# Optimization experiments

Measured on AMD Instinct MI355X. Metric: run time of the kernel, lower is better.

## Reference

```python
import jax, jax.numpy as jnp
import numpy as np

N = 100000
E = 1600000
DIN = 128
DOUT = 128
NUM_STEPS = 3


def setup_inputs() -> dict:
    key = jax.random.key(0)
    ks = jax.random.split(key, 12)
    stdv = 1.0 / np.sqrt(DOUT)
    xav = np.sqrt(6.0 / (2 * DOUT + DOUT))  # xavier_uniform for [DOUT, 2*DOUT]
    return {
        "input": jax.random.normal(ks[0], (N, DIN), dtype=jnp.float32),
        "edge_row": jax.random.randint(ks[1], (E,), 0, N, dtype=jnp.int32),
        "edge_col": jax.random.randint(ks[2], (E,), 0, N, dtype=jnp.int32),
        "edge_weight": jax.random.uniform(ks[3], (E,), dtype=jnp.float32),
        "weight": jax.random.uniform(ks[4], (DIN, DOUT), jnp.float32, -stdv, stdv),
        "bias": jax.random.uniform(ks[5], (DOUT,), jnp.float32, -stdv, stdv),
        "candidate_weight": jax.random.uniform(ks[6], (DOUT, DOUT), jnp.float32, -stdv, stdv),
        "ug_W": jax.random.uniform(ks[7], (DOUT, 2 * DOUT), jnp.float32, -xav, xav),
        "ug_b": jnp.zeros((DOUT,), jnp.float32),
        "rg_W": jax.random.uniform(ks[8], (DOUT, 2 * DOUT), jnp.float32, -xav, xav),
        "rg_b": jnp.zeros((DOUT,), jnp.float32),
    }


def reference(input, edge_row, edge_col, edge_weight, weight, bias,
              candidate_weight, ug_W, ug_b, rg_W, rg_b):
    n = input.shape[0]
    # h = input @ W + b
    h = input @ weight + bias
    for _ in range(NUM_STEPS):
        # spmm: m[dst] += w_e * h[src]
        msg = edge_weight[:, None] * h[edge_col]          # [E, DOUT]
        m = jax.ops.segment_sum(msg, edge_row, num_segments=n)  # [N, DOUT]
        g = jnp.concatenate([h, m], axis=1)               # [N, 2*DOUT]
        z = jax.nn.sigmoid(g @ ug_W.T + ug_b)
        r = jax.nn.sigmoid(g @ rg_W.T + rg_b)
        cand = jnp.tanh((r * h) @ candidate_weight)
        h = z * h + (1.0 - z) * cand
    return h
```

## Files before the change

kernel.cpp:

```cpp
#include <hip/hip_runtime.h>
#include <math.h>

#define NN 100000
#define EE 1600000
#define D 128
#define NBK 782
#define SBLK 128
#define EPB 12500
#define CAP 2304
#define EMAX 2048
#define INITB 3125

typedef __attribute__((ext_vector_type(8))) short short8;
typedef __attribute__((ext_vector_type(4))) float floatx4;

static __device__ __forceinline__ unsigned short f2bf(float f) {
  unsigned int u = __builtin_bit_cast(unsigned int, f);
  u = (u + 0x7fff + ((u >> 16) & 1)) >> 16;
  return (unsigned short)u;
}
static __device__ __forceinline__ unsigned int pk2(float a, float b) {
  return (unsigned int)f2bf(a) | ((unsigned int)f2bf(b) << 16);
}
static __device__ __forceinline__ float bflo(unsigned int u) { return __builtin_bit_cast(float, u << 16); }
static __device__ __forceinline__ float bfhi(unsigned int u) { return __builtin_bit_cast(float, u & 0xffff0000u); }
static __device__ __forceinline__ float bf2f(unsigned short s) {
  return __builtin_bit_cast(float, (unsigned int)s << 16);
}
static __device__ __forceinline__ float sig_f(float x) { return 1.f / (1.f + __expf(-x)); }
static __device__ __forceinline__ float tanh_f(float x) {
  float e = __expf(2.f * x);
  return 1.f - 2.f / (e + 1.f);
}
static __device__ __forceinline__ void fma8(float* acc, float w, uint4 h) {
  acc[0] += w * bflo(h.x); acc[1] += w * bfhi(h.x);
  acc[2] += w * bflo(h.y); acc[3] += w * bfhi(h.y);
  acc[4] += w * bflo(h.z); acc[5] += w * bfhi(h.z);
  acc[6] += w * bflo(h.w); acc[7] += w * bfhi(h.w);
}

__global__ __launch_bounds__(1024) void scatterpack(
    const int* __restrict__ erow, const int* __restrict__ ecol, const float* __restrict__ ew,
    int* __restrict__ len, int2* __restrict__ arena,
    const float* __restrict__ ugW, const float* __restrict__ rgW,
    const float* __restrict__ CW, const float* __restrict__ W,
    unsigned int* __restrict__ packZR, unsigned int* __restrict__ packCW,
    unsigned int* __restrict__ packW) {
  __shared__ int cur[NBK];
  const int tid = threadIdx.x;
  if (blockIdx.x < SBLK) {
    for (int b = tid; b < NBK; b += 1024) cur[b] = 0;
    __syncthreads();
    const int base = blockIdx.x * EPB;
    int r[13];
#pragma unroll
    for (int i = 0; i < 13; ++i) {
      int li = i * 1024 + tid;
      r[i] = (li < EPB) ? erow[base + li] : -1;
      if (r[i] >= 0) atomicAdd(&cur[r[i] >> 7], 1);
    }
    __syncthreads();
    for (int b = tid; b < NBK; b += 1024) {
      int c = cur[b];
      cur[b] = c ? (b * CAP + atomicAdd(&len[b], c)) : 0;
    }
    __syncthreads();
#pragma unroll
    for (int i = 0; i < 13; ++i) {
      if (r[i] >= 0) {
        int li = base + i * 1024 + tid;
        int pos = atomicAdd(&cur[r[i] >> 7], 1);
        int2 v;
        v.x = ecol[li] | ((r[i] & 127) << 24);
        v.y = __builtin_bit_cast(int, ew[li]);
        arena[pos] = v;
      }
    }
  } else {
    int g = (blockIdx.x - SBLK) * 16 + (tid >> 6);
    int lane = tid & 63;
    if (g < 128) {
      int nt = g >> 3, ks = g & 7;
      int o = nt * 16 + (lane & 15);
      int c0 = ks * 32 + (lane >> 4) * 8;
      const float* src = (o < 128 ? ugW + (size_t)o * 256 : rgW + (size_t)(o - 128) * 256) + c0;
      float4 f0 = ((const float4*)src)[0];
      float4 f1 = ((const float4*)src)[1];
      uint4 out;
      out.x = pk2(f0.x, f0.y);
      out.y = pk2(f0.z, f0.w);
      out.z = pk2(f1.x, f1.y);
      out.w = pk2(f1.z, f1.w);
      ((uint4*)packZR)[g * 64 + lane] = out;
    } else if (g < 192) {
      const float* M = (g < 160) ? CW : W;
      unsigned int* dst = (g < 160) ? packCW : packW;
      int gg = (g < 160) ? (g - 128) : (g - 160);
      int nt = gg >> 2, ks = gg & 3;
      int n = nt * 16 + (lane & 15);
      int k0 = ks * 32 + (lane >> 4) * 8;
      unsigned short v[8];
#pragma unroll
      for (int j = 0; j < 8; ++j) v[j] = f2bf(M[(size_t)(k0 + j) * 128 + n]);
      uint4 out;
      out.x = (unsigned int)v[0] | ((unsigned int)v[1] << 16);
      out.y = (unsigned int)v[2] | ((unsigned int)v[3] << 16);
      out.z = (unsigned int)v[4] | ((unsigned int)v[5] << 16);
      out.w = (unsigned int)v[6] | ((unsigned int)v[7] << 16);
      ((uint4*)dst)[gg * 64 + lane] = out;
    }
  }
}

__global__ __launch_bounds__(256) void sortinit(
    const int* __restrict__ len, int2* __restrict__ arena,
    int* __restrict__ row_start, int* __restrict__ row_end,
    const float* __restrict__ X, const short* __restrict__ packW, const float* __restrict__ bias,
    unsigned short* __restrict__ h_bf) {
  __shared__ __align__(16) char smem[CAP * 8 + 1024];
  const int tid = threadIdx.x;

  if (blockIdx.x < NBK) {
    int2* sE = (int2*)smem;
    int* rcnt = (int*)(smem + CAP * 8);
    int* rcur = rcnt + 128;
    const int b = blockIdx.x;
    const int lo = b * CAP;
    int n = len[b];
    n = (n < CAP) ? n : CAP;

    if (tid < 128) rcnt[tid] = 0;
    for (int i = tid; i < n; i += 256) sE[i] = arena[lo + i];
    __syncthreads();
    for (int i = tid; i < n; i += 256) atomicAdd(&rcnt[(sE[i].x >> 24) & 127], 1);
    __syncthreads();
    int myc = (tid < 128) ? rcnt[tid] : 0;
    for (int d = 1; d < 128; d <<= 1) {
      int v = (tid < 128 && tid >= d) ? rcnt[tid - d] : 0;
      __syncthreads();
      if (tid < 128) rcnt[tid] += v;
      __syncthreads();
    }
    if (tid < 128) {
      int excl = rcnt[tid] - myc;
      rcur[tid] = excl;
      int gr = b * 128 + tid;
      if (gr < NN) { row_start[gr] = lo + excl; row_end[gr] = lo + excl + myc; }
    }
    __syncthreads();
    for (int i = tid; i < n; i += 256) {
      int2 v = sE[i];
      int rl = (v.x >> 24) & 127;
      int pos = atomicAdd(&rcur[rl], 1);
      int2 o;
      o.x = v.x & 0x00FFFFFF;
      o.y = v.y;
      arena[lo + pos] = o;
    }
  } else {
    short* sX = (short*)smem;
    const int row0 = (blockIdx.x - NBK) * 32;

    {
      int r = tid >> 3, ch = tid & 7;
      const float4* px = (const float4*)(X + (size_t)(row0 + r) * D + ch * 16);
      float4 f0 = px[0], f1 = px[1], f2 = px[2], f3 = px[3];
      uint4 o0, o1;
      o0.x = pk2(f0.x, f0.y); o0.y = pk2(f0.z, f0.w);
      o0.z = pk2(f1.x, f1.y); o0.w = pk2(f1.z, f1.w);
      o1.x = pk2(f2.x, f2.y); o1.y = pk2(f2.z, f2.w);
      o1.z = pk2(f3.x, f3.y); o1.w = pk2(f3.z, f3.w);
      *(uint4*)(sX + r * 136 + ch * 16) = o0;
      *(uint4*)(sX + r * 136 + ch * 16 + 8) = o1;
    }
    __syncthreads();

    const int wave = tid >> 6, lane = tid & 63;
    const int quad = lane >> 4, l15 = lane & 15;
    const int mh = wave & 1, nh = wave >> 1;
    const int mrow = mh * 16 + l15;

    floatx4 acc[4];
    const floatx4 zero4 = {0.f, 0.f, 0.f, 0.f};
#pragma unroll
    for (int t = 0; t < 4; ++t) acc[t] = zero4;

    const short8* pW = (const short8*)packW;
#pragma unroll
    for (int ks = 0; ks < 4; ++ks) {
      short8 a = *(const short8*)(sX + mrow * 136 + ks * 32 + quad * 8);
#pragma unroll
      for (int t = 0; t < 4; ++t) {
        short8 b = pW[((nh * 4 + t) * 4 + ks) * 64 + lane];
        acc[t] = __builtin_amdgcn_mfma_f32_16x16x32_bf16(a, b, acc[t], 0, 0, 0);
      }
    }

    __syncthreads();
#pragma unroll
    for (int t = 0; t < 4; ++t) {
      int col = nh * 64 + t * 16 + l15;
      float bv = bias[col];
#pragma unroll
      for (int reg = 0; reg < 4; ++reg) {
        int row = mh * 16 + quad * 4 + reg;
        sX[row * 136 + col] = (short)f2bf(acc[t][reg] + bv);
      }
    }
    __syncthreads();
    for (int idx = tid; idx < 512; idx += 256) {
      int r = idx >> 4, ch = idx & 15;
      *(uint4*)(h_bf + (size_t)(row0 + r) * D + ch * 8) = *(uint4*)(sX + r * 136 + ch * 8);
    }
  }
}

__global__ __launch_bounds__(512, 8) void fused_step(
    const int* __restrict__ row_start, const int* __restrict__ row_end,
    const int2* __restrict__ edata,
    const uint4* __restrict__ h4,
    const short* __restrict__ packZR, const short* __restrict__ packCW,
    const float* __restrict__ ugb, const float* __restrict__ rgb,
    unsigned short* __restrict__ h_bf_out, float* __restrict__ h_f32_out, int last) {
  __shared__ __align__(16) short sA[32 * 264];
  __shared__ __align__(16) char sU[EMAX * 8];
  int2* sE = (int2*)sU;
  short* sRH = (short*)sU;

  const int tid = threadIdx.x;
  const int row0 = blockIdx.x * 32;
  const int wave = tid >> 6, lane = tid & 63;
  const int sub = lane >> 4, li = lane & 15;

  {
    int r = tid >> 4, ch = tid & 15;
    *(uint4*)(sA + r * 264 + ch * 8) = h4[(size_t)(row0 + r) * 16 + ch];
  }

  const int myrow = row0 + wave * 4 + sub;
  const int rs0 = row_start[myrow];
  const int rs1 = row_end[myrow];
  const int seg_lo = row_start[row0];
  const int seg_hi = row_end[row0 + 31];

  float acc[8];
#pragma unroll
  for (int j = 0; j < 8; ++j) acc[j] = 0.f;

  for (int clo = seg_lo; clo < seg_hi; clo += EMAX) {
    const int chi = min(clo + EMAX, seg_hi);
    for (int i = clo + tid; i < chi; i += 512) sE[i - clo] = edata[i];
    __syncthreads();

    int kb = max(rs0, clo) - clo;
    int ke = min(rs1, chi) - clo;
    for (; kb + 2 <= ke; kb += 2) {
      int2 e0 = sE[kb];
      int2 e1 = sE[kb + 1];
      uint4 h0 = h4[(size_t)e0.x * 16 + li];
      uint4 h1 = h4[(size_t)e1.x * 16 + li];
      fma8(acc, __builtin_bit_cast(float, e0.y), h0);
      fma8(acc, __builtin_bit_cast(float, e1.y), h1);
    }
    if (kb < ke) {
      int2 e0 = sE[kb];
      uint4 h0 = h4[(size_t)e0.x * 16 + li];
      fma8(acc, __builtin_bit_cast(float, e0.y), h0);
    }
    __syncthreads();
  }

  {
    uint4 o;
    o.x = pk2(acc[0], acc[1]);
    o.y = pk2(acc[2], acc[3]);
    o.z = pk2(acc[4], acc[5]);
    o.w = pk2(acc[6], acc[7]);
    *(uint4*)(sA + (wave * 4 + sub) * 264 + 128 + li * 8) = o;
  }
  __syncthreads();

  const int quad = lane >> 4, l15 = lane & 15;
  const int mh = wave >> 2, nh = wave & 3;
  const int mrow = mh * 16 + l15;

  floatx4 accZ[2], accR[2];
  const floatx4 zero4 = {0.f, 0.f, 0.f, 0.f};
#pragma unroll
  for (int t = 0; t < 2; ++t) { accZ[t] = zero4; accR[t] = zero4; }

  const short8* pB = (const short8*)packZR;
#pragma unroll
  for (int ks = 0; ks < 8; ++ks) {
    short8 a = *(const short8*)(sA + mrow * 264 + ks * 32 + quad * 8);
#pragma unroll
    for (int t = 0; t < 2; ++t) {
      short8 bz = pB[((nh * 2 + t) * 8 + ks) * 64 + lane];
      accZ[t] = __builtin_amdgcn_mfma_f32_16x16x32_bf16(a, bz, accZ[t], 0, 0, 0);
      short8 br = pB[((8 + nh * 2 + t) * 8 + ks) * 64 + lane];
      accR[t] = __builtin_amdgcn_mfma_f32_16x16x32_bf16(a, br, accR[t], 0, 0, 0);
    }
  }

#pragma unroll
  for (int t = 0; t < 2; ++t) {
    int col = nh * 32 + t * 16 + l15;
    float zb = ugb[col], rb = rgb[col];
#pragma unroll
    for (int reg = 0; reg < 4; ++reg) {
      int row = mh * 16 + quad * 4 + reg;
      float z = sig_f(accZ[t][reg] + zb);
      float rr = sig_f(accR[t][reg] + rb);
      float hv = bf2f((unsigned short)sA[row * 264 + col]);
      sRH[row * 136 + col] = (short)f2bf(rr * hv);
      accZ[t][reg] = z;
    }
  }
  __syncthreads();

  floatx4 acc2[2];
#pragma unroll
  for (int t = 0; t < 2; ++t) acc2[t] = zero4;

  const short8* pC = (const short8*)packCW;
#pragma unroll
  for (int ks = 0; ks < 4; ++ks) {
    short8 a = *(const short8*)(sRH + mrow * 136 + ks * 32 + quad * 8);
#pragma unroll
    for (int t = 0; t < 2; ++t) {
      short8 b = pC[((nh * 2 + t) * 4 + ks) * 64 + lane];
      acc2[t] = __builtin_amdgcn_mfma_f32_16x16x32_bf16(a, b, acc2[t], 0, 0, 0);
    }
  }

#pragma unroll
  for (int t = 0; t < 2; ++t) {
    int col = nh * 32 + t * 16 + l15;
#pragma unroll
    for (int reg = 0; reg < 4; ++reg) {
      int row = mh * 16 + quad * 4 + reg;
      float cand = tanh_f(acc2[t][reg]);
      float z = accZ[t][reg];
      float hold = bf2f((unsigned short)sA[row * 264 + col]);
      float hn = z * hold + (1.f - z) * cand;
      if (last) h_f32_out[(size_t)(row0 + row) * D + col] = hn;
      else sA[row * 264 + col] = (short)f2bf(hn);
    }
  }
  if (!last) {
    __syncthreads();
    int r = tid >> 4, ch = tid & 15;
    *(uint4*)(h_bf_out + (size_t)(row0 + r) * D + ch * 8) = *(uint4*)(sA + r * 264 + ch * 8);
  }
}

extern "C" void kernel_launch(void* const* d_in, const int* in_sizes, int n_in,
                              void* d_out, int out_size, void* d_ws, size_t ws_size,
                              hipStream_t stream) {
  const float* input = (const float*)d_in[0];
  const int* erow    = (const int*)d_in[1];
  const int* ecol    = (const int*)d_in[2];
  const float* ew    = (const float*)d_in[3];
  const float* W     = (const float*)d_in[4];
  const float* bias  = (const float*)d_in[5];
  const float* CW    = (const float*)d_in[6];
  const float* ugW   = (const float*)d_in[7];
  const float* ugb   = (const float*)d_in[8];
  const float* rgW   = (const float*)d_in[9];
  const float* rgb   = (const float*)d_in[10];

  float* h_out = (float*)d_out;

  char* ws = (char*)d_ws;
  unsigned short* hA = (unsigned short*)ws;   ws += (size_t)NN * D * 2;
  unsigned short* hB = (unsigned short*)ws;   ws += (size_t)NN * D * 2;
  unsigned int* packZR = (unsigned int*)ws;   ws += 16 * 8 * 64 * 16;
  unsigned int* packCW = (unsigned int*)ws;   ws += 8 * 4 * 64 * 16;
  unsigned int* packW  = (unsigned int*)ws;   ws += 8 * 4 * 64 * 16;
  int2* arena    = (int2*)ws;                 ws += (size_t)NBK * CAP * sizeof(int2);
  int* len       = (int*)ws;                  ws += NBK * sizeof(int);
  int* row_start = (int*)ws;                  ws += NN * sizeof(int);
  int* row_end   = (int*)ws;                  ws += NN * sizeof(int);

  hipMemsetAsync(len, 0, NBK * sizeof(int), stream);
  scatterpack<<<SBLK + 12, 1024, 0, stream>>>(erow, ecol, ew, len, arena,
                                              ugW, rgW, CW, W, packZR, packCW, packW);
  sortinit<<<NBK + INITB, 256, 0, stream>>>(len, arena, row_start, row_end,
                                            input, (const short*)packW, bias, hA);

  fused_step<<<NN / 32, 512, 0, stream>>>(row_start, row_end, arena, (const uint4*)hA,
                                          (const short*)packZR, (const short*)packCW,
                                          ugb, rgb, hB, h_out, 0);
  fused_step<<<NN / 32, 512, 0, stream>>>(row_start, row_end, arena, (const uint4*)hB,
                                          (const short*)packZR, (const short*)packCW,
                                          ugb, rgb, hA, h_out, 0);
  fused_step<<<NN / 32, 512, 0, stream>>>(row_start, row_end, arena, (const uint4*)hA,
                                          (const short*)packZR, (const short*)packCW,
                                          ugb, rgb, hB, h_out, 1);
}
```

Measured before the change: 477.0 us.

## Regroup preprocessing: pack weights first, overlap scatter with input projection, separate sort

The preprocessing pipeline is reorganized. Weight packing and zeroing of the bucket counters now happen in a small first kernel, replacing the memset. Edge scattering then runs in the same launch as the initial input projection, which is batched four 32-row tiles per 1024-thread block. The per-bucket sort moves to its own kernel. The launch count stays the same, but the aim is to overlap the atomic-heavy scatter with the MFMA projection instead of running the projection alongside the sort. The cost is one extra dependent launch boundary, plus larger blocks that may reduce occupancy for the projection.

```diff
diff --git a/kernel.cpp b/kernel.cpp
--- a/kernel.cpp
+++ b/kernel.cpp
@@ -10,6 +10,7 @@
 #define CAP 2304
 #define EMAX 2048
 #define INITB 3125
+#define IBLK 782
 
 typedef __attribute__((ext_vector_type(8))) short short8;
 typedef __attribute__((ext_vector_type(4))) float floatx4;
@@ -39,16 +40,56 @@
   acc[6] += w * bflo(h.w); acc[7] += w * bfhi(h.w);
 }
 
-__global__ __launch_bounds__(1024) void scatterpack(
-    const int* __restrict__ erow, const int* __restrict__ ecol, const float* __restrict__ ew,
-    int* __restrict__ len, int2* __restrict__ arena,
+__global__ __launch_bounds__(64) void packzero(
     const float* __restrict__ ugW, const float* __restrict__ rgW,
     const float* __restrict__ CW, const float* __restrict__ W,
     unsigned int* __restrict__ packZR, unsigned int* __restrict__ packCW,
-    unsigned int* __restrict__ packW) {
-  __shared__ int cur[NBK];
+    unsigned int* __restrict__ packW, int* __restrict__ len) {
+  int lane = threadIdx.x;
+  if (blockIdx.x < 128) {
+    int g = blockIdx.x;
+    int nt = g >> 3, ks = g & 7;
+    int o = nt * 16 + (lane & 15);
+    int c0 = ks * 32 + (lane >> 4) * 8;
+    const float* src = (o < 128 ? ugW + (size_t)o * 256 : rgW + (size_t)(o - 128) * 256) + c0;
+    float4 f0 = ((const float4*)src)[0];
+    float4 f1 = ((const float4*)src)[1];
+    uint4 out;
+    out.x = pk2(f0.x, f0.y);
+    out.y = pk2(f0.z, f0.w);
+    out.z = pk2(f1.x, f1.y);
+    out.w = pk2(f1.z, f1.w);
+    ((uint4*)packZR)[g * 64 + lane] = out;
+  } else if (blockIdx.x < 192) {
+    const float* M = (blockIdx.x < 160) ? CW : W;
+    unsigned int* dst = (blockIdx.x < 160) ? packCW : packW;
+    int g = (blockIdx.x - 128) & 31;
+    int nt = g >> 2, ks = g & 3;
+    int n = nt * 16 + (lane & 15);
+    int k0 = ks * 32 + (lane >> 4) * 8;
+    unsigned short v[8];
+#pragma unroll
+    for (int j = 0; j < 8; ++j) v[j] = f2bf(M[(size_t)(k0 + j) * 128 + n]);
+    uint4 out;
+    out.x = (unsigned int)v[0] | ((unsigned int)v[1] << 16);
+    out.y = (unsigned int)v[2] | ((unsigned int)v[3] << 16);
+    out.z = (unsigned int)v[4] | ((unsigned int)v[5] << 16);
+    out.w = (unsigned int)v[6] | ((unsigned int)v[7] << 16);
+    ((uint4*)dst)[g * 64 + lane] = out;
+  } else {
+    for (int b = lane; b < NBK; b += 64) len[b] = 0;
+  }
+}
+
+__global__ __launch_bounds__(1024) void scatinit(
+    const int* __restrict__ erow, const int* __restrict__ ecol, const float* __restrict__ ew,
+    int* __restrict__ len, int2* __restrict__ arena,
+    const float* __restrict__ X, const short* __restrict__ packW, const float* __restrict__ bias,
+    unsigned short* __restrict__ h_bf) {
+  __shared__ __align__(16) char sm[34816];
   const int tid = threadIdx.x;
   if (blockIdx.x < SBLK) {
+    int* cur = (int*)sm;
     for (int b = tid; b < NBK; b += 1024) cur[b] = 0;
     __syncthreads();
     const int base = blockIdx.x * EPB;
@@ -77,92 +118,14 @@
       }
     }
   } else {
-    int g = (blockIdx.x - SBLK) * 16 + (tid >> 6);
-    int lane = tid & 63;
-    if (g < 128) {
-      int nt = g >> 3, ks = g & 7;
-      int o = nt * 16 + (lane & 15);
-      int c0 = ks * 32 + (lane >> 4) * 8;
-      const float* src = (o < 128 ? ugW + (size_t)o * 256 : rgW + (size_t)(o - 128) * 256) + c0;
-      float4 f0 = ((const float4*)src)[0];
-      float4 f1 = ((const float4*)src)[1];
-      uint4 out;
-      out.x = pk2(f0.x, f0.y);
-      out.y = pk2(f0.z, f0.w);
-      out.z = pk2(f1.x, f1.y);
-      out.w = pk2(f1.z, f1.w);
-      ((uint4*)packZR)[g * 64 + lane] = out;
-    } else if (g < 192) {
-      const float* M = (g < 160) ? CW : W;
-      unsigned int* dst = (g < 160) ? packCW : packW;
-      int gg = (g < 160) ? (g - 128) : (g - 160);
-      int nt = gg >> 2, ks = gg & 3;
-      int n = nt * 16 + (lane & 15);
-      int k0 = ks * 32 + (lane >> 4) * 8;
-      unsigned short v[8];
-#pragma unroll
-      for (int j = 0; j < 8; ++j) v[j] = f2bf(M[(size_t)(k0 + j) * 128 + n]);
-      uint4 out;
-      out.x = (unsigned int)v[0] | ((unsigned int)v[1] << 16);
-      out.y = (unsigned int)v[2] | ((unsigned int)v[3] << 16);
-      out.z = (unsigned int)v[4] | ((unsigned int)v[5] << 16);
-      out.w = (unsigned int)v[6] | ((unsigned int)v[7] << 16);
-      ((uint4*)dst)[gg * 64 + lane] = out;
-    }
-  }
-}
-
-__global__ __launch_bounds__(256) void sortinit(
-    const int* __restrict__ len, int2* __restrict__ arena,
-    int* __restrict__ row_start, int* __restrict__ row_end,
-    const float* __restrict__ X, const short* __restrict__ packW, const float* __restrict__ bias,
-    unsigned short* __restrict__ h_bf) {
-  __shared__ __align__(16) char smem[CAP * 8 + 1024];
-  const int tid = threadIdx.x;
-
-  if (blockIdx.x < NBK) {
-    int2* sE = (int2*)smem;
-    int* rcnt = (int*)(smem + CAP * 8);
-    int* rcur = rcnt + 128;
-    const int b = blockIdx.x;
-    const int lo = b * CAP;
-    int n = len[b];
-    n = (n < CAP) ? n : CAP;
-
-    if (tid < 128) rcnt[tid] = 0;
-    for (int i = tid; i < n; i += 256) sE[i] = arena[lo + i];
-    __syncthreads();
-    for (int i = tid; i < n; i += 256) atomicAdd(&rcnt[(sE[i].x >> 24) & 127], 1);
-    __syncthreads();
-    int myc = (tid < 128) ? rcnt[tid] : 0;
-    for (int d = 1; d < 128; d <<= 1) {
-      int v = (tid < 128 && tid >= d) ? rcnt[tid - d] : 0;
-      __syncthreads();
-      if (tid < 128) rcnt[tid] += v;
-      __syncthreads();
-    }
-    if (tid < 128) {
-      int excl = rcnt[tid] - myc;
-      rcur[tid] = excl;
-      int gr = b * 128 + tid;
-      if (gr < NN) { row_start[gr] = lo + excl; row_end[gr] = lo + excl + myc; }
-    }
-    __syncthreads();
-    for (int i = tid; i < n; i += 256) {
-      int2 v = sE[i];
-      int rl = (v.x >> 24) & 127;
-      int pos = atomicAdd(&rcur[rl], 1);
-      int2 o;
-      o.x = v.x & 0x00FFFFFF;
-      o.y = v.y;
-      arena[lo + pos] = o;
-    }
-  } else {
-    short* sX = (short*)smem;
-    const int row0 = (blockIdx.x - NBK) * 32;
+    short* sX = (short*)(sm + (tid >> 8) * 8704);
+    const int t = tid & 255;
+    const int tile = (blockIdx.x - SBLK) * 4 + (tid >> 8);
+    const bool valid = (tile < INITB);
+    const int row0 = valid ? tile * 32 : 0;
 
     {
-      int r = tid >> 3, ch = tid & 7;
+      int r = t >> 3, ch = t & 7;
       const float4* px = (const float4*)(X + (size_t)(row0 + r) * D + ch * 16);
       float4 f0 = px[0], f1 = px[1], f2 = px[2], f3 = px[3];
       uint4 o0, o1;
@@ -175,7 +138,7 @@
     }
     __syncthreads();
 
-    const int wave = tid >> 6, lane = tid & 63;
+    const int wave = (t >> 6), lane = tid & 63;
     const int quad = lane >> 4, l15 = lane & 15;
     const int mh = wave & 1, nh = wave >> 1;
     const int mrow = mh * 16 + l15;
@@ -183,35 +146,79 @@
     floatx4 acc[4];
     const floatx4 zero4 = {0.f, 0.f, 0.f, 0.f};
 #pragma unroll
-    for (int t = 0; t < 4; ++t) acc[t] = zero4;
+    for (int tt = 0; tt < 4; ++tt) acc[tt] = zero4;
 
     const short8* pW = (const short8*)packW;
 #pragma unroll
     for (int ks = 0; ks < 4; ++ks) {
       short8 a = *(const short8*)(sX + mrow * 136 + ks * 32 + quad * 8);
 #pragma unroll
-      for (int t = 0; t < 4; ++t) {
-        short8 b = pW[((nh * 4 + t) * 4 + ks) * 64 + lane];
-        acc[t] = __builtin_amdgcn_mfma_f32_16x16x32_bf16(a, b, acc[t], 0, 0, 0);
+      for (int tt = 0; tt < 4; ++tt) {
+        short8 b = pW[((nh * 4 + tt) * 4 + ks) * 64 + lane];
+        acc[tt] = __builtin_amdgcn_mfma_f32_16x16x32_bf16(a, b, acc[tt], 0, 0, 0);
       }
     }
 
     __syncthreads();
 #pragma unroll
-    for (int t = 0; t < 4; ++t) {
-      int col = nh * 64 + t * 16 + l15;
+    for (int tt = 0; tt < 4; ++tt) {
+      int col = nh * 64 + tt * 16 + l15;
       float bv = bias[col];
 #pragma unroll
       for (int reg = 0; reg < 4; ++reg) {
         int row = mh * 16 + quad * 4 + reg;
-        sX[row * 136 + col] = (short)f2bf(acc[t][reg] + bv);
+        sX[row * 136 + col] = (short)f2bf(acc[tt][reg] + bv);
       }
     }
     __syncthreads();
-    for (int idx = tid; idx < 512; idx += 256) {
-      int r = idx >> 4, ch = idx & 15;
-      *(uint4*)(h_bf + (size_t)(row0 + r) * D + ch * 8) = *(uint4*)(sX + r * 136 + ch * 8);
-    }
+    if (valid) {
+      int r = t >> 3, ch0 = (t & 7) * 2;
+      *(uint4*)(h_bf + (size_t)(row0 + r) * D + ch0 * 8) = *(uint4*)(sX + r * 136 + ch0 * 8);
+      *(uint4*)(h_bf + (size_t)(row0 + r) * D + ch0 * 8 + 8) = *(uint4*)(sX + r * 136 + ch0 * 8 + 8);
+    }
+  }
+}
+
+__global__ __launch_bounds__(256) void b_sortk(
+    const int* __restrict__ len, int2* __restrict__ arena,
+    int* __restrict__ row_start, int* __restrict__ row_end) {
+  __shared__ __align__(16) char smem[CAP * 8 + 1024];
+  int2* sE = (int2*)smem;
+  int* rcnt = (int*)(smem + CAP * 8);
+  int* rcur = rcnt + 128;
+  const int tid = threadIdx.x;
+  const int b = blockIdx.x;
+  const int lo = b * CAP;
+  int n = len[b];
+  n = (n < CAP) ? n : CAP;
+
+  if (tid < 128) rcnt[tid] = 0;
+  for (int i = tid; i < n; i += 256) sE[i] = arena[lo + i];
+  __syncthreads();
+  for (int i = tid; i < n; i += 256) atomicAdd(&rcnt[(sE[i].x >> 24) & 127], 1);
+  __syncthreads();
+  int myc = (tid < 128) ? rcnt[tid] : 0;
+  for (int d = 1; d < 128; d <<= 1) {
+    int v = (tid < 128 && tid >= d) ? rcnt[tid - d] : 0;
+    __syncthreads();
+    if (tid < 128) rcnt[tid] += v;
+    __syncthreads();
+  }
+  if (tid < 128) {
+    int excl = rcnt[tid] - myc;
+    rcur[tid] = excl;
+    int gr = b * 128 + tid;
+    if (gr < NN) { row_start[gr] = lo + excl; row_end[gr] = lo + excl + myc; }
+  }
+  __syncthreads();
+  for (int i = tid; i < n; i += 256) {
+    int2 v = sE[i];
+    int rl = (v.x >> 24) & 127;
+    int pos = atomicAdd(&rcur[rl], 1);
+    int2 o;
+    o.x = v.x & 0x00FFFFFF;
+    o.y = v.y;
+    arena[lo + pos] = o;
   }
 }
 
@@ -382,11 +389,10 @@
   int* row_start = (int*)ws;                  ws += NN * sizeof(int);
   int* row_end   = (int*)ws;                  ws += NN * sizeof(int);
 
-  hipMemsetAsync(len, 0, NBK * sizeof(int), stream);
-  scatterpack<<<SBLK + 12, 1024, 0, stream>>>(erow, ecol, ew, len, arena,
-                                              ugW, rgW, CW, W, packZR, packCW, packW);
-  sortinit<<<NBK + INITB, 256, 0, stream>>>(len, arena, row_start, row_end,
-                                            input, (const short*)packW, bias, hA);
+  packzero<<<193, 64, 0, stream>>>(ugW, rgW, CW, W, packZR, packCW, packW, len);
+  scatinit<<<SBLK + IBLK, 1024, 0, stream>>>(erow, ecol, ew, len, arena,
+                                             input, (const short*)packW, bias, hA);
+  b_sortk<<<NBK, 256, 0, stream>>>(len, arena, row_start, row_end);
 
   fused_step<<<NN / 32, 512, 0, stream>>>(row_start, row_end, arena, (const uint4*)hA,
                                           (const short*)packZR, (const short*)packCW,
```

Result: no change. 473.4 us (-0.7%).
